# Kernel optimization log

Hardware: AMD Instinct MI355X
Metric: run time of the kernel (lower is better)

Reference implementation:

```python
import jax, jax.numpy as jnp
import numpy as np

NF = 64   # node features
EF = 5    # edge types
AEF = 8   # attention edge types
MF = 64   # message features
B = 16
N = 64


def setup_inputs() -> dict:
    key = jax.random.key(0)
    k1, k2, k3, k4, k5 = jax.random.split(key, 5)
    afm = jax.random.normal(k1, (B, N, NF), dtype=jnp.float32)
    bfm = jax.random.randint(k2, (B, N, N), 0, EF + 1)          # 0 = no edge
    a_bfm = jax.random.randint(k3, (B, N), 0, AEF + 1)          # 0 = no attention
    # kaiming-uniform-like init
    adj_w = jax.random.uniform(k4, (EF, MF, NF), jnp.float32, -1.0, 1.0) * np.sqrt(6.0 / NF)
    adj_a = jax.random.uniform(k5, (AEF, MF), jnp.float32, -1.0, 1.0) * np.sqrt(6.0 / MF)
    message_bias = jnp.zeros((MF,), dtype=jnp.float32)
    return {"afm": afm, "bfm": bfm, "a_bfm": a_bfm,
            "adj_w": adj_w, "adj_a": adj_a, "message_bias": message_bias}


def reference(afm, bfm, a_bfm, adj_w, adj_a, message_bias):
    mf, nf = adj_w.shape[1], adj_w.shape[2]
    # prepend zero entry so index 0 means "no edge" / "no attention"
    w_full = jnp.concatenate([jnp.zeros((1, mf, nf), adj_w.dtype), adj_w], axis=0)   # (EF+1, mf, nf)
    a_full = jnp.concatenate([jnp.zeros((1, mf), adj_a.dtype), adj_a], axis=0)       # (AEF+1, mf)
    # gather per-edge weight blocks: (B, N, N, mf, nf)
    edge_w = w_full[bfm]
    # block matmul: messages[b,i,m] = sum_{j,n} W[type(b,i,j), m, n] * afm[b,j,n]
    msg = jnp.einsum('bijmn,bjn->bim', edge_w, afm)
    # per-row attention scaling (commutes with the contraction over j,n)
    att = a_full[a_bfm]                                                               # (B, N, mf)
    return msg * att + message_bias
```

## Files before the change

kernel.cpp:

```cpp
#include <hip/hip_runtime.h>

#define NB  16
#define NN  64
#define NFD 64
#define EFD 5
#define MFD 64
#define THREADS 256

typedef const __attribute__((address_space(1))) void* gas_ptr;
typedef __attribute__((address_space(3))) void*       las_ptr;

__global__ __launch_bounds__(THREADS)
void ggnn_msgpass_kernel(const float* __restrict__ afm,
                         const int*   __restrict__ bfm,
                         const int*   __restrict__ a_bfm,
                         const float* __restrict__ adj_w,
                         const float* __restrict__ adj_a,
                         const float* __restrict__ bias,
                         float* __restrict__ out)
{
    __shared__ float afm_s[NN * NFD];
    __shared__ float W_s[EFD * MFD * NFD];

    const int t    = threadIdx.x;
    const int lane = t & 63;
    const int g    = t >> 6;
    const int bx   = blockIdx.x;
    const int b    = bx >> 4;
    const int i    = ((bx & 15) << 2) + g;

    {
        const float4* wsrc = (const float4*)adj_w;
#pragma unroll
        for (int k = 0; k < 20; ++k) {
            int q = g * 20 + k;
            __builtin_amdgcn_global_load_lds((gas_ptr)(wsrc + q * 64 + lane),
                                             (las_ptr)(W_s + q * 256),
                                             16, 0, 0);
        }
        const float4* asrc = (const float4*)(afm + (size_t)b * NN * NFD);
#pragma unroll
        for (int k = 0; k < 4; ++k) {
            int q = g * 4 + k;
            __builtin_amdgcn_global_load_lds((gas_ptr)(asrc + q * 64 + lane),
                                             (las_ptr)(afm_s + q * 256),
                                             16, 0, 0);
        }
    }

    const int   bfm_reg = bfm[((size_t)b * NN + i) * NN + lane];
    const int   a       = a_bfm[b * NN + i];
    const float bv      = bias[lane];

    __syncthreads();

    const float att = (a > 0) ? adj_a[(size_t)(a - 1) * MFD + lane] : 0.f;

    float ac0 = 0.f, ac1 = 0.f, ac2 = 0.f, ac3 = 0.f, ac4 = 0.f;
#pragma unroll
    for (int j = 0; j < NN; ++j) {
        float v = afm_s[j * NFD + lane];
        int e = __builtin_amdgcn_readlane(bfm_reg, j);
        ac0 = fmaf((e == 1) ? 1.f : 0.f, v, ac0);
        ac1 = fmaf((e == 2) ? 1.f : 0.f, v, ac1);
        ac2 = fmaf((e == 3) ? 1.f : 0.f, v, ac2);
        ac3 = fmaf((e == 4) ? 1.f : 0.f, v, ac3);
        ac4 = fmaf((e == 5) ? 1.f : 0.f, v, ac4);
    }

    float p[MFD];
#pragma unroll
    for (int m = 0; m < MFD; ++m) {
        const float* wb = W_s + (size_t)m * NFD + lane;
        float w0 = wb[0 * MFD * NFD];
        float w1 = wb[1 * MFD * NFD];
        float w2 = wb[2 * MFD * NFD];
        float w3 = wb[3 * MFD * NFD];
        float w4 = wb[4 * MFD * NFD];
        p[m] = w0 * ac0 + w1 * ac1 + w2 * ac2 + w3 * ac3 + w4 * ac4;
    }

#pragma unroll
    for (int s = 32; s >= 1; s >>= 1) {
#pragma unroll
        for (int m = 0; m < s; ++m) {
            float lo = p[m], hi = p[m + s];
            bool upper  = (lane & s) != 0;
            float mine  = upper ? hi : lo;
            float other = upper ? lo : hi;
            float recv  = __shfl_xor(other, s, 64);
            p[m] = mine + recv;
        }
    }
    float r = p[0];

    out[((size_t)b * NN + i) * MFD + lane] = r * att + bv;
}

extern "C" void kernel_launch(void* const* d_in, const int* in_sizes, int n_in,
                              void* d_out, int out_size, void* d_ws, size_t ws_size,
                              hipStream_t stream) {
    const float* afm   = (const float*)d_in[0];
    const int*   bfm   = (const int*)d_in[1];
    const int*   a_bfm = (const int*)d_in[2];
    const float* adj_w = (const float*)d_in[3];
    const float* adj_a = (const float*)d_in[4];
    const float* bias  = (const float*)d_in[5];
    float* out = (float*)d_out;

    dim3 grid(NB * (NN / 4));
    dim3 block(THREADS);
    ggnn_msgpass_kernel<<<grid, block, 0, stream>>>(afm, bfm, a_bfm, adj_w,
                                                    adj_a, bias, out);
}
```

Before: 69.95 us.

## Tile blocks over 16 rows by 16 message features to cut weight staging

Each block now handles 16 output rows and a 16-wide slice of message features, instead of 4 rows and all 64 features. Every wavefront processes 4 rows, so each weight value loaded from shared memory is reused across 4 rows. Only a quarter of the weight tensor is staged per block, which cuts per-block LDS traffic and footprint (about 20KB of weights instead of 80KB). The cost is 20 accumulators per thread plus a 64-entry partial array, which raises register pressure. The edge-type accumulation loop also does 4x the readlane and select work per wavefront.

```diff
diff --git a/kernel.cpp b/kernel.cpp
--- a/kernel.cpp
+++ b/kernel.cpp
@@ -20,22 +20,26 @@
                          float* __restrict__ out)
 {
     __shared__ float afm_s[NN * NFD];
-    __shared__ float W_s[EFD * MFD * NFD];
+    __shared__ float W_s[EFD * 16 * NFD];
 
     const int t    = threadIdx.x;
     const int lane = t & 63;
     const int g    = t >> 6;
     const int bx   = blockIdx.x;
     const int b    = bx >> 4;
-    const int i    = ((bx & 15) << 2) + g;
+    const int i0   = ((bx & 15) >> 2) * 16;
+    const int mb   = (bx & 3) * 16;
+    const int ir   = i0 + g * 4;
 
     {
         const float4* wsrc = (const float4*)adj_w;
 #pragma unroll
-        for (int k = 0; k < 20; ++k) {
-            int q = g * 20 + k;
-            __builtin_amdgcn_global_load_lds((gas_ptr)(wsrc + q * 64 + lane),
-                                             (las_ptr)(W_s + q * 256),
+        for (int k = 0; k < 5; ++k) {
+            int q  = g * 5 + k;
+            int e  = q >> 2, mg = q & 3;
+            int sf4 = e * 1024 + mb * 16 + mg * 64;
+            __builtin_amdgcn_global_load_lds((gas_ptr)(wsrc + sf4 + lane),
+                                             (las_ptr)(W_s + e * 1024 + mg * 256),
                                              16, 0, 0);
         }
         const float4* asrc = (const float4*)(afm + (size_t)b * NN * NFD);
@@ -48,36 +52,51 @@
         }
     }
 
-    const int   bfm_reg = bfm[((size_t)b * NN + i) * NN + lane];
-    const int   a       = a_bfm[b * NN + i];
-    const float bv      = bias[lane];
+    int bfm_reg[4];
+#pragma unroll
+    for (int r = 0; r < 4; ++r)
+        bfm_reg[r] = bfm[((size_t)b * NN + ir + r) * NN + lane];
+
+    const int   a_e  = a_bfm[b * NN + ir + (lane >> 4)];
+    const float bv   = bias[mb + (lane & 15)];
 
     __syncthreads();
 
-    const float att = (a > 0) ? adj_a[(size_t)(a - 1) * MFD + lane] : 0.f;
+    const float att = (a_e > 0) ? adj_a[(size_t)(a_e - 1) * MFD + mb + (lane & 15)]
+                                : 0.f;
 
-    float ac0 = 0.f, ac1 = 0.f, ac2 = 0.f, ac3 = 0.f, ac4 = 0.f;
+    float ac[4][EFD];
+#pragma unroll
+    for (int r = 0; r < 4; ++r)
+#pragma unroll
+        for (int e = 0; e < EFD; ++e) ac[r][e] = 0.f;
+
 #pragma unroll
     for (int j = 0; j < NN; ++j) {
         float v = afm_s[j * NFD + lane];
-        int e = __builtin_amdgcn_readlane(bfm_reg, j);
-        ac0 = fmaf((e == 1) ? 1.f : 0.f, v, ac0);
-        ac1 = fmaf((e == 2) ? 1.f : 0.f, v, ac1);
-        ac2 = fmaf((e == 3) ? 1.f : 0.f, v, ac2);
-        ac3 = fmaf((e == 4) ? 1.f : 0.f, v, ac3);
-        ac4 = fmaf((e == 5) ? 1.f : 0.f, v, ac4);
+#pragma unroll
+        for (int r = 0; r < 4; ++r) {
+            int e = __builtin_amdgcn_readlane(bfm_reg[r], j);
+            ac[r][0] = fmaf((e == 1) ? 1.f : 0.f, v, ac[r][0]);
+            ac[r][1] = fmaf((e == 2) ? 1.f : 0.f, v, ac[r][1]);
+            ac[r][2] = fmaf((e == 3) ? 1.f : 0.f, v, ac[r][2]);
+            ac[r][3] = fmaf((e == 4) ? 1.f : 0.f, v, ac[r][3]);
+            ac[r][4] = fmaf((e == 5) ? 1.f : 0.f, v, ac[r][4]);
+        }
     }
 
-    float p[MFD];
+    float p[64];
 #pragma unroll
-    for (int m = 0; m < MFD; ++m) {
-        const float* wb = W_s + (size_t)m * NFD + lane;
-        float w0 = wb[0 * MFD * NFD];
-        float w1 = wb[1 * MFD * NFD];
-        float w2 = wb[2 * MFD * NFD];
-        float w3 = wb[3 * MFD * NFD];
-        float w4 = wb[4 * MFD * NFD];
-        p[m] = w0 * ac0 + w1 * ac1 + w2 * ac2 + w3 * ac3 + w4 * ac4;
+    for (int ml = 0; ml < 16; ++ml) {
+        float w0 = W_s[0 * 1024 + ml * NFD + lane];
+        float w1 = W_s[1 * 1024 + ml * NFD + lane];
+        float w2 = W_s[2 * 1024 + ml * NFD + lane];
+        float w3 = W_s[3 * 1024 + ml * NFD + lane];
+        float w4 = W_s[4 * 1024 + ml * NFD + lane];
+#pragma unroll
+        for (int r = 0; r < 4; ++r)
+            p[r * 16 + ml] = w0 * ac[r][0] + w1 * ac[r][1] + w2 * ac[r][2]
+                           + w3 * ac[r][3] + w4 * ac[r][4];
     }
 
 #pragma unroll
@@ -94,7 +113,7 @@
     }
     float r = p[0];
 
-    out[((size_t)b * NN + i) * MFD + lane] = r * att + bv;
+    out[((size_t)b * NN + ir + (lane >> 4)) * MFD + mb + (lane & 15)] = r * att + bv;
 }
 
 extern "C" void kernel_launch(void* const* d_in, const int* in_sizes, int n_in,
@@ -108,7 +127,7 @@
     const float* bias  = (const float*)d_in[5];
     float* out = (float*)d_out;
 
-    dim3 grid(NB * (NN / 4));
+    dim3 grid(256);
     dim3 block(THREADS);
     ggnn_msgpass_kernel<<<grid, block, 0, stream>>>(afm, bfm, a_bfm, adj_w,
                                                     adj_a, bias, out);
```

After: 75.94 us. +8.6%, slower.

## Split weight matrix across warps by output rows and share accumulators via LDS

Applied to the files above, without the earlier changes.

Each block no longer stages the full 80 KB weight tensor in shared memory. Each wavefront now loads only its 16 output rows for all 5 edge types (80 values) into registers straight from global memory. The per-row edge-type accumulators are exchanged through a small LDS buffer so every wavefront can compute 16 outputs for all 4 rows, and the output index mapping is changed to match. This cuts LDS footprint and bulk copy traffic, which should raise occupancy, at the cost of 80 extra registers per thread, uncoalesced-ish global reads, and one additional barrier.

```diff
diff --git a/kernel.cpp b/kernel.cpp
--- a/kernel.cpp
+++ b/kernel.cpp
@@ -20,24 +20,17 @@
                          float* __restrict__ out)
 {
     __shared__ float afm_s[NN * NFD];
-    __shared__ float W_s[EFD * MFD * NFD];
+    __shared__ float ac_s[4][EFD][NFD];
 
     const int t    = threadIdx.x;
     const int lane = t & 63;
     const int g    = t >> 6;
     const int bx   = blockIdx.x;
     const int b    = bx >> 4;
-    const int i    = ((bx & 15) << 2) + g;
+    const int i0   = (bx & 15) << 2;
+    const int i    = i0 + g;
 
     {
-        const float4* wsrc = (const float4*)adj_w;
-#pragma unroll
-        for (int k = 0; k < 20; ++k) {
-            int q = g * 20 + k;
-            __builtin_amdgcn_global_load_lds((gas_ptr)(wsrc + q * 64 + lane),
-                                             (las_ptr)(W_s + q * 256),
-                                             16, 0, 0);
-        }
         const float4* asrc = (const float4*)(afm + (size_t)b * NN * NFD);
 #pragma unroll
         for (int k = 0; k < 4; ++k) {
@@ -49,12 +42,18 @@
     }
 
     const int   bfm_reg = bfm[((size_t)b * NN + i) * NN + lane];
-    const int   a       = a_bfm[b * NN + i];
-    const float bv      = bias[lane];
+    const int   a_row = a_bfm[b * NN + i0 + (lane >> 4)];
+    const float bv    = bias[g * 16 + (lane & 15)];
+    const float att   = (a_row > 0)
+                      ? adj_a[(size_t)(a_row - 1) * MFD + g * 16 + (lane & 15)]
+                      : 0.f;
 
     __syncthreads();
 
-    const float att = (a > 0) ? adj_a[(size_t)(a - 1) * MFD + lane] : 0.f;
+    float wv[80];
+#pragma unroll
+    for (int p = 0; p < 80; ++p)
+        wv[p] = adj_w[(size_t)(p / 16) * MFD * NFD + (g * 16 + (p % 16)) * NFD + lane];
 
     float ac0 = 0.f, ac1 = 0.f, ac2 = 0.f, ac3 = 0.f, ac4 = 0.f;
 #pragma unroll
@@ -67,18 +66,31 @@
         ac3 = fmaf((e == 4) ? 1.f : 0.f, v, ac3);
         ac4 = fmaf((e == 5) ? 1.f : 0.f, v, ac4);
     }
+    ac_s[g][0][lane] = ac0;
+    ac_s[g][1][lane] = ac1;
+    ac_s[g][2][lane] = ac2;
+    ac_s[g][3][lane] = ac3;
+    ac_s[g][4][lane] = ac4;
 
-    float p[MFD];
+    __syncthreads();
+
+    float acr[4][EFD];
 #pragma unroll
-    for (int m = 0; m < MFD; ++m) {
-        const float* wb = W_s + (size_t)m * NFD + lane;
-        float w0 = wb[0 * MFD * NFD];
-        float w1 = wb[1 * MFD * NFD];
-        float w2 = wb[2 * MFD * NFD];
-        float w3 = wb[3 * MFD * NFD];
-        float w4 = wb[4 * MFD * NFD];
-        p[m] = w0 * ac0 + w1 * ac1 + w2 * ac2 + w3 * ac3 + w4 * ac4;
-    }
+    for (int r = 0; r < 4; ++r)
+#pragma unroll
+        for (int e = 0; e < EFD; ++e)
+            acr[r][e] = ac_s[r][e][lane];
+
+    float p[64];
+#pragma unroll
+    for (int r = 0; r < 4; ++r)
+#pragma unroll
+        for (int ml = 0; ml < 16; ++ml)
+            p[r * 16 + ml] = wv[0 * 16 + ml] * acr[r][0]
+                           + wv[1 * 16 + ml] * acr[r][1]
+                           + wv[2 * 16 + ml] * acr[r][2]
+                           + wv[3 * 16 + ml] * acr[r][3]
+                           + wv[4 * 16 + ml] * acr[r][4];
 
 #pragma unroll
     for (int s = 32; s >= 1; s >>= 1) {
@@ -92,9 +104,10 @@
             p[m] = mine + recv;
         }
     }
-    float r = p[0];
+    float res = p[0];
 
-    out[((size_t)b * NN + i) * MFD + lane] = r * att + bv;
+    out[((size_t)b * NN + i0 + (lane >> 4)) * MFD + g * 16 + (lane & 15)]
+        = res * att + bv;
 }
 
 extern "C" void kernel_launch(void* const* d_in, const int* in_sizes, int n_in,
@@ -108,7 +121,7 @@
     const float* bias  = (const float*)d_in[5];
     float* out = (float*)d_out;
 
-    dim3 grid(NB * (NN / 4));
+    dim3 grid(256);
     dim3 block(THREADS);
     ggnn_msgpass_kernel<<<grid, block, 0, stream>>>(afm, bfm, a_bfm, adj_w,
                                                     adj_a, bias, out);
```

Result: faster. 67.79 us (-3.1%).
